# Performance work log

Measured on AMD Instinct MI355X. Metric: run time of the kernel, lower is better.

The kernel has to match this reference:

```python
import jax, jax.numpy as jnp
from jax import lax
import numpy as np

B, C, H, W = 8, 1024, 32, 32
M = 32768
EPS = 1e-12  # clamp before sqrt, matching typical torch euclidean_dist


def setup_inputs() -> dict:
    key = jax.random.key(0)
    k1, k2 = jax.random.split(key)
    features = jax.random.normal(k1, (B, C, H, W), dtype=jnp.float32)
    coreset = jax.random.normal(k2, (M, C), dtype=jnp.float32)
    return {"features": features, "coreset": coreset}


def reference(features, coreset):
    # F.avg_pool2d(features, 3, 1, 1): kernel 3, stride 1, pad 1,
    # count_include_pad=True (torch default) -> window sum / 9.
    pooled = lax.reduce_window(
        features, jnp.float32(0.0), lax.add,
        window_dimensions=(1, 1, 3, 3),
        window_strides=(1, 1, 1, 1),
        padding=((0, 0), (0, 0), (1, 1), (1, 1)),
    ) / jnp.float32(9.0)
    # permute(0,2,3,1).view(B, H*W, C) then flatten batch -> [N, C]
    emb = pooled.transpose(0, 2, 3, 1).reshape(-1, C)  # [N=B*H*W, C]
    x2 = jnp.sum(emb * emb, axis=-1, keepdims=True)        # [N, 1]
    y2 = jnp.sum(coreset * coreset, axis=-1)               # [M]
    d2 = x2 + y2[None, :] - 2.0 * (emb @ coreset.T)        # [N, M]
    dist = jnp.sqrt(jnp.clip(d2, EPS))
    min_dist = jnp.min(dist, axis=1)                       # [N] 1-NN distance
    return min_dist
```

## Files before the change

kernel.cpp:

```cpp
#include <hip/hip_runtime.h>
#include <stdint.h>
#include <math.h>


#define N_TOT 8192
#define M_TOT 32768
#define C_TOT 1024
#define EPS_ 1e-12f

typedef short bf16x8 __attribute__((ext_vector_type(8)));
typedef float f32x4 __attribute__((ext_vector_type(4)));

__device__ __forceinline__ unsigned short f2bf_rne(float f) {
    unsigned u = __float_as_uint(f);
    u += 0x7fffu + ((u >> 16) & 1u);
    return (unsigned short)(u >> 16);
}
__device__ __forceinline__ float bf2f(unsigned short h) {
    return __uint_as_float(((unsigned)h) << 16);
}

__global__ void init_kernel(unsigned* __restrict__ d2u, float* __restrict__ x2) {
    int i = blockIdx.x * blockDim.x + threadIdx.x;
    if (i < N_TOT) { d2u[i] = 0x7F800000u; x2[i] = 0.0f; }
}

__global__ __launch_bounds__(256) void pool_kernel(const float* __restrict__ feat,
                                                   unsigned short* __restrict__ emb,
                                                   float* __restrict__ x2) {
    int bid = blockIdx.x;
    int h  = bid & 31;
    int cc = (bid >> 5) & 31;
    int b  = bid >> 10;
    int tid = threadIdx.x;
    __shared__ float lds[32 * 97];

    const float* base = feat + ((size_t)(b * 1024 + cc * 32)) * 1024;
    int g0 = (h - 1) * 32;
    #pragma unroll
    for (int it = 0; it < 12; ++it) {
        int e = tid + it * 256;
        int ci = e / 96;
        int j  = e - ci * 96;
        int g  = g0 + j;
        float v = 0.0f;
        if (g >= 0 && g < 1024) v = base[(size_t)ci * 1024 + g];
        lds[ci * 97 + j] = v;
    }
    __syncthreads();

    int c  = tid & 31;
    int wb = tid >> 5;
    const float inv9 = 1.0f / 9.0f;
    #pragma unroll
    for (int i = 0; i < 4; ++i) {
        int w = wb + i * 8;
        float s = 0.0f;
        #pragma unroll
        for (int rr = 0; rr < 3; ++rr) {
            int rb = c * 97 + rr * 32 + w;
            s += lds[rb];
            if (w > 0)  s += lds[rb - 1];
            if (w < 31) s += lds[rb + 1];
        }
        float p = s * inv9;
        unsigned short bh = f2bf_rne(p);
        int n = b * 1024 + h * 32 + w;
        emb[(size_t)n * 1024 + cc * 32 + c] = bh;
        float pf = bf2f(bh);
        float sq = pf * pf;
        #pragma unroll
        for (int off = 1; off < 32; off <<= 1) sq += __shfl_xor(sq, off);
        if (c == 0) atomicAdd(&x2[n], sq);
    }
}

__global__ __launch_bounds__(256) void cs_kernel(const float* __restrict__ cs,
                                                 unsigned short* __restrict__ csb,
                                                 float* __restrict__ y2) {
    int row = blockIdx.x;
    int tid = threadIdx.x;
    float4 v = reinterpret_cast<const float4*>(cs + (size_t)row * 1024)[tid];
    ushort4 o;
    o.x = f2bf_rne(v.x); o.y = f2bf_rne(v.y);
    o.z = f2bf_rne(v.z); o.w = f2bf_rne(v.w);
    reinterpret_cast<ushort4*>(csb + (size_t)row * 1024)[tid] = o;
    float a = bf2f(o.x), b = bf2f(o.y), c = bf2f(o.z), d = bf2f(o.w);
    float s = a * a + b * b + c * c + d * d;
    #pragma unroll
    for (int off = 1; off < 64; off <<= 1) s += __shfl_xor(s, off);
    __shared__ float red[4];
    if ((tid & 63) == 0) red[tid >> 6] = s;
    __syncthreads();
    if (tid == 0) y2[row] = red[0] + red[1] + red[2] + red[3];
}

__global__ __launch_bounds__(256) void gemm_min_kernel(const unsigned short* __restrict__ emb,
                                                       const unsigned short* __restrict__ csb,
                                                       const float* __restrict__ x2,
                                                       const float* __restrict__ y2,
                                                       unsigned* __restrict__ d2u) {
    int bid = blockIdx.x;
    int xcd   = bid & 7;
    int local = bid >> 3;
    int st    = local >> 6;
    int idx   = local & 63;
    int si = idx >> 3;
    int sj = idx & 7;
    int in = (st & 7) * 8 + si;
    int im = xcd * 32 + (st >> 3) * 8 + sj;
    int nb = in * 128;
    int mb = im * 128;

    int tid  = threadIdx.x;
    int lane = tid & 63;
    int wid  = tid >> 6;
    int wr = wid >> 1, wc = wid & 1;

    __shared__ unsigned short lds[8192];
    unsigned short* lA = lds;
    unsigned short* lB = lds + 4096;

    f32x4 acc[4][4];
    #pragma unroll
    for (int m = 0; m < 4; ++m)
        #pragma unroll
        for (int n = 0; n < 4; ++n) acc[m][n] = (f32x4){0.f, 0.f, 0.f, 0.f};

    const unsigned short* gA = emb + (size_t)nb * 1024;
    const unsigned short* gB = csb + (size_t)mb * 1024;

    int fr = lane & 15;
    int kq = lane >> 4;

    for (int kt = 0; kt < 32; ++kt) {
        int k0 = kt * 32;
        __syncthreads();
        #pragma unroll
        for (int i = 0; i < 2; ++i) {
            int seg = i * 256 + wid * 64 + lane;
            int row = seg >> 2;
            int ks  = seg & 3;
            __builtin_amdgcn_global_load_lds(
                (__attribute__((address_space(1))) void*)(gA + (size_t)row * 1024 + k0 + ks * 8),
                (__attribute__((address_space(3))) void*)(lA + (i * 256 + wid * 64) * 8),
                16, 0, 0);
            __builtin_amdgcn_global_load_lds(
                (__attribute__((address_space(1))) void*)(gB + (size_t)row * 1024 + k0 + ks * 8),
                (__attribute__((address_space(3))) void*)(lB + (i * 256 + wid * 64) * 8),
                16, 0, 0);
        }
        __syncthreads();

        bf16x8 af[4], bfv[4];
        #pragma unroll
        for (int m = 0; m < 4; ++m)
            af[m] = *reinterpret_cast<const bf16x8*>(&lA[(wr * 64 + m * 16 + fr) * 32 + kq * 8]);
        #pragma unroll
        for (int n = 0; n < 4; ++n)
            bfv[n] = *reinterpret_cast<const bf16x8*>(&lB[(wc * 64 + n * 16 + fr) * 32 + kq * 8]);
        #pragma unroll
        for (int m = 0; m < 4; ++m)
            #pragma unroll
            for (int n = 0; n < 4; ++n)
                acc[m][n] = __builtin_amdgcn_mfma_f32_16x16x32_bf16(af[m], bfv[n], acc[m][n], 0, 0, 0);
    }

    int cc = lane & 15;
    int rq = (lane >> 4) * 4;
    float y2v[4];
    #pragma unroll
    for (int n = 0; n < 4; ++n) y2v[n] = y2[mb + wc * 64 + n * 16 + cc];

    #pragma unroll
    for (int m = 0; m < 4; ++m) {
        #pragma unroll
        for (int j = 0; j < 4; ++j) {
            float v = y2v[0] - 2.0f * acc[m][0][j];
            #pragma unroll
            for (int n = 1; n < 4; ++n) v = fminf(v, y2v[n] - 2.0f * acc[m][n][j]);
            int grow = nb + wr * 64 + m * 16 + rq + j;
            float d2 = x2[grow] + v;
            d2 = fmaxf(d2, EPS_);
            #pragma unroll
            for (int off = 1; off < 16; off <<= 1) d2 = fminf(d2, __shfl_xor(d2, off));
            if (cc == 0) atomicMin(&d2u[grow], __float_as_uint(d2));
        }
    }
}

__global__ void sqrt_kernel(const unsigned* __restrict__ d2u, float* __restrict__ out) {
    int i = blockIdx.x * blockDim.x + threadIdx.x;
    if (i < N_TOT) out[i] = sqrtf(__uint_as_float(d2u[i]));
}

extern "C" void kernel_launch(void* const* d_in, const int* in_sizes, int n_in,
                              void* d_out, int out_size, void* d_ws, size_t ws_size,
                              hipStream_t stream) {
    const float* feat = (const float*)d_in[0];
    const float* cs   = (const float*)d_in[1];
    float* out = (float*)d_out;

    char* ws = (char*)d_ws;
    unsigned short* emb = (unsigned short*)ws;
    unsigned short* csb = (unsigned short*)(ws + 16777216);
    float* x2 = (float*)(ws + 16777216 + 67108864);
    float* y2 = x2 + N_TOT;
    unsigned* d2u = (unsigned*)(y2 + M_TOT);

    init_kernel<<<N_TOT / 256, 256, 0, stream>>>(d2u, x2);
    pool_kernel<<<8192, 256, 0, stream>>>(feat, emb, x2);
    cs_kernel<<<M_TOT, 256, 0, stream>>>(cs, csb, y2);
    gemm_min_kernel<<<16384, 256, 0, stream>>>(emb, csb, x2, y2, d2u);
    sqrt_kernel<<<N_TOT / 256, 256, 0, stream>>>(d2u, out);
}
```

Before: 951.9 us.

## Rewrite GEMM-min as 256x256 tiles with triple-buffered LDS pipeline and swizzle

The distance GEMM moves from 128x128 tiles on 256 threads to 256x256 tiles on 512 threads, with each wave computing a 128x64 sub-tile. Global-to-LDS loads are triple-buffered and prefetched two k-steps ahead, synchronised by explicit vmcnt waits and barriers. LDS chunks are XOR-swizzled to reduce bank conflicts, and MFMA sections run at raised priority. The aim is to hide load latency and raise operand reuse per byte loaded. The cost is 96 KB of LDS and more accumulator registers per block, which lowers occupancy.

```diff
diff --git a/kernel.cpp b/kernel.cpp
--- a/kernel.cpp
+++ b/kernel.cpp
@@ -5,8 +5,8 @@
 
 #define N_TOT 8192
 #define M_TOT 32768
-#define C_TOT 1024
 #define EPS_ 1e-12f
+#define S_KT 32
 
 typedef short bf16x8 __attribute__((ext_vector_type(8)));
 typedef float f32x4 __attribute__((ext_vector_type(4)));
@@ -95,91 +95,115 @@
     if (tid == 0) y2[row] = red[0] + red[1] + red[2] + red[3];
 }
 
-__global__ __launch_bounds__(256) void gemm_min_kernel(const unsigned short* __restrict__ emb,
-                                                       const unsigned short* __restrict__ csb,
-                                                       const float* __restrict__ x2,
-                                                       const float* __restrict__ y2,
-                                                       unsigned* __restrict__ d2u) {
+
+#define STAGE(BUF, TT) do {                                                              \
+    int t_ = (TT);                                                                       \
+    _Pragma("unroll")                                                                    \
+    for (int s_ = 0; s_ < 2; ++s_) {                                                     \
+        __builtin_amdgcn_global_load_lds(                                                \
+            (const __attribute__((address_space(1))) void*)(gA + (size_t)(s_ * 128 + rowq) * 1024 + t_ * 32 + ch * 8), \
+            (__attribute__((address_space(3))) void*)(&lds[(BUF) * 16384 + s_ * 4096 + tid * 8]), 16, 0, 0); \
+        __builtin_amdgcn_global_load_lds(                                                \
+            (const __attribute__((address_space(1))) void*)(gB + (size_t)(s_ * 128 + rowq) * 1024 + t_ * 32 + ch * 8), \
+            (__attribute__((address_space(3))) void*)(&lds[(BUF) * 16384 + 8192 + s_ * 4096 + tid * 8]), 16, 0, 0); \
+    }                                                                                    \
+} while (0)
+
+#define DS_MFMA(BCUR) do {                                                               \
+    bf16x8 af[8], bv[4];                                                                 \
+    const unsigned short* pA = &lds[(BCUR) * 16384 + (wmBase + fr) * 32 + sx];           \
+    const unsigned short* pB = &lds[(BCUR) * 16384 + 8192 + (wnBase + fr) * 32 + sx];    \
+    _Pragma("unroll")                                                                    \
+    for (int m = 0; m < 8; ++m) af[m] = *reinterpret_cast<const bf16x8*>(pA + m * 512);  \
+    _Pragma("unroll")                                                                    \
+    for (int n = 0; n < 4; ++n) bv[n] = *reinterpret_cast<const bf16x8*>(pB + n * 512);  \
+    asm volatile("s_waitcnt lgkmcnt(0)" ::: "memory");                                   \
+    __builtin_amdgcn_s_barrier();                                                        \
+    __builtin_amdgcn_s_setprio(1);                                                       \
+    _Pragma("unroll")                                                                    \
+    for (int m = 0; m < 8; ++m)                                                          \
+        _Pragma("unroll")                                                                \
+        for (int n = 0; n < 4; ++n)                                                      \
+            acc[m][n] = __builtin_amdgcn_mfma_f32_16x16x32_bf16(af[m], bv[n], acc[m][n], 0, 0, 0); \
+    __builtin_amdgcn_s_setprio(0);                                                       \
+} while (0)
+
+#define GEMM_ITER(BCUR, BSTG, TN) do {                                                   \
+    STAGE(BSTG, TN);                                                                     \
+    asm volatile("s_waitcnt vmcnt(8)" ::: "memory");                                     \
+    __builtin_amdgcn_s_barrier();                                                        \
+    DS_MFMA(BCUR);                                                                       \
+} while (0)
+
+__global__ __launch_bounds__(512, 2) void gemm_min_kernel(const unsigned short* __restrict__ emb,
+                                                          const unsigned short* __restrict__ csb,
+                                                          const float* __restrict__ x2,
+                                                          const float* __restrict__ y2,
+                                                          unsigned* __restrict__ d2u) {
+    __shared__ unsigned short lds[49152];
+
     int bid = blockIdx.x;
     int xcd   = bid & 7;
     int local = bid >> 3;
-    int st    = local >> 6;
-    int idx   = local & 63;
-    int si = idx >> 3;
-    int sj = idx & 7;
-    int in = (st & 7) * 8 + si;
-    int im = xcd * 32 + (st >> 3) * 8 + sj;
-    int nb = in * 128;
-    int mb = im * 128;
+    int st    = local >> 4;
+    int idx   = local & 15;
+    int si = idx >> 2, sj = idx & 3;
+    int emb_tile = (st & 7) * 4 + si;
+    int cs_tile  = xcd * 16 + (st >> 3) * 4 + sj;
+    int nb = emb_tile * 256;
+    int mb = cs_tile * 256;
 
     int tid  = threadIdx.x;
     int lane = tid & 63;
     int wid  = tid >> 6;
-    int wr = wid >> 1, wc = wid & 1;
-
-    __shared__ unsigned short lds[8192];
-    unsigned short* lA = lds;
-    unsigned short* lB = lds + 4096;
-
-    f32x4 acc[4][4];
-    #pragma unroll
-    for (int m = 0; m < 4; ++m)
-        #pragma unroll
-        for (int n = 0; n < 4; ++n) acc[m][n] = (f32x4){0.f, 0.f, 0.f, 0.f};
-
+    int wmBase = (wid >> 2) * 128;
+    int wnBase = (wid & 3) * 64;
+
+    int rowq = tid >> 2;
+    int ch   = (tid & 3) ^ ((tid >> 3) & 3);
     const unsigned short* gA = emb + (size_t)nb * 1024;
     const unsigned short* gB = csb + (size_t)mb * 1024;
 
     int fr = lane & 15;
     int kq = lane >> 4;
-
-    for (int kt = 0; kt < 32; ++kt) {
-        int k0 = kt * 32;
-        __syncthreads();
-        #pragma unroll
-        for (int i = 0; i < 2; ++i) {
-            int seg = i * 256 + wid * 64 + lane;
-            int row = seg >> 2;
-            int ks  = seg & 3;
-            __builtin_amdgcn_global_load_lds(
-                (__attribute__((address_space(1))) void*)(gA + (size_t)row * 1024 + k0 + ks * 8),
-                (__attribute__((address_space(3))) void*)(lA + (i * 256 + wid * 64) * 8),
-                16, 0, 0);
-            __builtin_amdgcn_global_load_lds(
-                (__attribute__((address_space(1))) void*)(gB + (size_t)row * 1024 + k0 + ks * 8),
-                (__attribute__((address_space(3))) void*)(lB + (i * 256 + wid * 64) * 8),
-                16, 0, 0);
-        }
-        __syncthreads();
-
-        bf16x8 af[4], bfv[4];
-        #pragma unroll
-        for (int m = 0; m < 4; ++m)
-            af[m] = *reinterpret_cast<const bf16x8*>(&lA[(wr * 64 + m * 16 + fr) * 32 + kq * 8]);
-        #pragma unroll
-        for (int n = 0; n < 4; ++n)
-            bfv[n] = *reinterpret_cast<const bf16x8*>(&lB[(wc * 64 + n * 16 + fr) * 32 + kq * 8]);
-        #pragma unroll
-        for (int m = 0; m < 4; ++m)
-            #pragma unroll
-            for (int n = 0; n < 4; ++n)
-                acc[m][n] = __builtin_amdgcn_mfma_f32_16x16x32_bf16(af[m], bfv[n], acc[m][n], 0, 0, 0);
-    }
+    int sx = (kq ^ ((fr >> 1) & 3)) * 8;
+
+    f32x4 acc[8][4];
+    #pragma unroll
+    for (int m = 0; m < 8; ++m)
+        #pragma unroll
+        for (int n = 0; n < 4; ++n) acc[m][n] = (f32x4){0.f, 0.f, 0.f, 0.f};
+
+    STAGE(0, 0);
+    STAGE(1, 1);
+
+    #pragma unroll 1
+    for (int u = 0; u < 30; u += 3) {
+        GEMM_ITER(0, 2, u + 2);
+        GEMM_ITER(1, 0, u + 3);
+        GEMM_ITER(2, 1, u + 4);
+    }
+    asm volatile("s_waitcnt vmcnt(4)" ::: "memory");
+    __builtin_amdgcn_s_barrier();
+    DS_MFMA(0);
+    asm volatile("s_waitcnt vmcnt(0)" ::: "memory");
+    __builtin_amdgcn_s_barrier();
+    DS_MFMA(1);
 
     int cc = lane & 15;
     int rq = (lane >> 4) * 4;
     float y2v[4];
     #pragma unroll
-    for (int n = 0; n < 4; ++n) y2v[n] = y2[mb + wc * 64 + n * 16 + cc];
-
-    #pragma unroll
-    for (int m = 0; m < 4; ++m) {
+    for (int n = 0; n < 4; ++n) y2v[n] = y2[mb + wnBase + n * 16 + cc];
+
+    #pragma unroll
+    for (int m = 0; m < 8; ++m) {
         #pragma unroll
         for (int j = 0; j < 4; ++j) {
             float v = y2v[0] - 2.0f * acc[m][0][j];
             #pragma unroll
             for (int n = 1; n < 4; ++n) v = fminf(v, y2v[n] - 2.0f * acc[m][n][j]);
-            int grow = nb + wr * 64 + m * 16 + rq + j;
+            int grow = nb + wmBase + m * 16 + rq + j;
             float d2 = x2[grow] + v;
             d2 = fmaxf(d2, EPS_);
             #pragma unroll
@@ -211,6 +235,6 @@
     init_kernel<<<N_TOT / 256, 256, 0, stream>>>(d2u, x2);
     pool_kernel<<<8192, 256, 0, stream>>>(feat, emb, x2);
     cs_kernel<<<M_TOT, 256, 0, stream>>>(cs, csb, y2);
-    gemm_min_kernel<<<16384, 256, 0, stream>>>(emb, csb, x2, y2, d2u);
+    gemm_min_kernel<<<4096, 512, 0, stream>>>(emb, csb, x2, y2, d2u);
     sqrt_kernel<<<N_TOT / 256, 256, 0, stream>>>(d2u, out);
 }
```

Result: faster. 885.6 us (-7.0%).
